# Performance work log

Hardware: AMD Instinct MI355X
Metric: run time of the kernel (lower is better)

## Reference

```python
import jax, jax.numpy as jnp
import numpy as np

TEMPERATURE = 0.07


def setup_inputs() -> dict:
    key = jax.random.key(0)
    k1, k2, k3 = jax.random.split(key, 3)
    B, V, D = 512, 1, 512
    features = jax.random.normal(k1, (B, V, D), dtype=jnp.float32)
    mask = jax.random.randint(k2, (B, B), 0, 2).astype(jnp.float32)
    mask_sents = jax.random.randint(k3, (B,), 0, 2).astype(jnp.bool_)
    return {"features": features, "mask": mask, "mask_sents": mask_sents}


def reference(features, mask, mask_sents):
    # features: [B, 1, D]; mask: [B, B] (0/1); mask_sents: [B] bool anchor selector
    B = features.shape[0]
    anchor = features[:, 0]                     # contrast_count == 1 -> anchor == contrast
    sim = jnp.matmul(anchor, anchor.T) / TEMPERATURE   # [B, B]

    logits_mask = 1.0 - jnp.eye(B, dtype=sim.dtype)    # zero out self-comparison
    sel = mask_sents.astype(sim.dtype)[:, None]        # weight instead of boolean row-select
    mask_pos = mask * logits_mask * sel                # [B, B]
    mask_neg = (1.0 - mask) * logits_mask * sel        # [B, B]

    # 'pre' branch: sum over rows i and (pos p, neg n) pairs of -logsigmoid(sim[i,p]-sim[i,n])
    diff = sim[:, :, None] - sim[:, None, :]           # [B, P, N] pairwise differences
    neg_logsig = -jax.nn.log_sigmoid(diff)
    loss_sum = jnp.einsum('ipn,ip,in->', neg_logsig, mask_pos, mask_neg)
    pair_num = jnp.sum(mask_pos.sum(1) * mask_neg.sum(1))
    loss = jnp.where(pair_num > 0, loss_sum / jnp.maximum(pair_num, 1.0), loss_sum)
    return loss
```

## Files before the change

kernel.cpp:

```cpp
#include <hip/hip_runtime.h>
#include <hip/hip_bf16.h>
#include <math.h>

#define BDIM 512
#define DDIM 512
#define SPLIT 4

typedef __attribute__((ext_vector_type(8))) short bfrag;
typedef __attribute__((ext_vector_type(4))) float ffrag;

__global__ __launch_bounds__(256) void convert_bf16(const float* __restrict__ A,
                                                    __hip_bfloat16* __restrict__ Ab,
                                                    double* __restrict__ acc) {
    const int idx = (blockIdx.x * 256 + threadIdx.x) * 4;
    if (idx == 0) { acc[0] = 0.0; acc[1] = 0.0; }
    float4 v = *(const float4*)&A[idx];
    union { __hip_bfloat16 h[4]; ushort4 u; } cv;
    cv.h[0] = __float2bfloat16(v.x); cv.h[1] = __float2bfloat16(v.y);
    cv.h[2] = __float2bfloat16(v.z); cv.h[3] = __float2bfloat16(v.w);
    *(ushort4*)&Ab[idx] = cv.u;
}

__global__ __launch_bounds__(256) void gemm_mfma(const __hip_bfloat16* __restrict__ Ab,
                                                 float* __restrict__ S) {
    const int tid = threadIdx.x;
    const int w = tid >> 6, lane = tid & 63;
    const int quad = lane >> 4, r = lane & 15;
    const int m0 = blockIdx.y * 64 + w * 16;
    const int n0 = blockIdx.x * 16;
    const __hip_bfloat16* arow = Ab + (m0 + r) * DDIM + quad * 8;
    const __hip_bfloat16* brow = Ab + (n0 + r) * DDIM + quad * 8;
    ffrag acc = {0.f, 0.f, 0.f, 0.f};
#pragma unroll
    for (int k = 0; k < DDIM; k += 32) {
        bfrag af = *(const bfrag*)(arow + k);
        bfrag bf = *(const bfrag*)(brow + k);
        acc = __builtin_amdgcn_mfma_f32_16x16x32_bf16(af, bf, acc, 0, 0, 0);
    }
    const float sc = 1.0f / 0.07f;
#pragma unroll
    for (int rg = 0; rg < 4; ++rg)
        S[(m0 + quad * 4 + rg) * BDIM + n0 + r] = acc[rg] * sc;
}

__device__ __forceinline__ float softplus_f(float z) {
    return fmaxf(z, 0.0f) + __logf(1.0f + __expf(-fabsf(z)));
}

__global__ __launch_bounds__(256) void pair_loss(const float* __restrict__ S,
                                                 const float* __restrict__ mask,
                                                 const int* __restrict__ sel,
                                                 double* __restrict__ acc) {
    const int i = blockIdx.x >> 2;
    const int q = blockIdx.x & 3;
    if (sel[i] == 0) return;
    __shared__ float sm[BDIM];
    __shared__ __align__(16) float ps[BDIM + 4];
    __shared__ float ns[BDIM];
    __shared__ int cnt[2];
    __shared__ float wsum[4];
    const int tid = threadIdx.x;
    const int lane = tid & 63, wave = tid >> 6;
    if (tid < 2) cnt[tid] = 0;
    for (int p = tid; p < BDIM; p += 256) sm[p] = S[i * BDIM + p];
    __syncthreads();
#pragma unroll
    for (int r = 0; r < 2; ++r) {
        const int p = tid + r * 256;
        const float m = mask[i * BDIM + p];
        const bool ok  = (p != i);
        const bool isp = ok && (m != 0.0f);
        const bool isn = ok && (m == 0.0f);
        unsigned long long bp = __ballot(isp);
        unsigned long long bn = __ballot(isn);
        unsigned long long lower = (1ULL << lane) - 1ULL;
        int pbase = 0, nbase = 0;
        if (lane == 0) {
            pbase = atomicAdd(&cnt[0], __popcll(bp));
            nbase = atomicAdd(&cnt[1], __popcll(bn));
        }
        pbase = __shfl(pbase, 0, 64);
        nbase = __shfl(nbase, 0, 64);
        if (isp) ps[pbase + __popcll(bp & lower)] = sm[p];
        if (isn) ns[nbase + __popcll(bn & lower)] = sm[p];
    }
    __syncthreads();
    const int npos = cnt[0], nneg = cnt[1];
    if (tid < 4) ps[npos + tid] = INFINITY;
    __syncthreads();
    int p0 = (q == 0) ? 0 : min(npos, ((q * npos) / SPLIT + 3) & ~3);
    int p1 = (q == SPLIT - 1) ? npos : min(npos, (((q + 1) * npos) / SPLIT + 3) & ~3);
    float l0 = 0.f, l1 = 0.f, l2 = 0.f, l3 = 0.f;
    for (int pp = p0; pp < p1; pp += 4) {
        float4 sp = *(const float4*)&ps[pp];
        for (int nn = tid; nn < nneg; nn += 256) {
            float sn = ns[nn];
            l0 += softplus_f(sn - sp.x);
            l1 += softplus_f(sn - sp.y);
            l2 += softplus_f(sn - sp.z);
            l3 += softplus_f(sn - sp.w);
        }
    }
    float local = (l0 + l1) + (l2 + l3);
#pragma unroll
    for (int off = 32; off > 0; off >>= 1) local += __shfl_down(local, off, 64);
    if (lane == 0) wsum[wave] = local;
    __syncthreads();
    if (tid == 0) {
        double tot = (double)wsum[0] + (double)wsum[1] + (double)wsum[2] + (double)wsum[3];
        atomicAdd(&acc[0], tot);
        if (q == 0) atomicAdd(&acc[1], (double)npos * (double)nneg);
    }
}

__global__ void finalize(const double* __restrict__ acc, float* __restrict__ out) {
    double ls = acc[0], pn = acc[1];
    double loss = (pn > 0.0) ? ls / fmax(pn, 1.0) : ls;
    out[0] = (float)loss;
}

extern "C" void kernel_launch(void* const* d_in, const int* in_sizes, int n_in,
                              void* d_out, int out_size, void* d_ws, size_t ws_size,
                              hipStream_t stream) {
    const float* feat = (const float*)d_in[0];
    const float* mask = (const float*)d_in[1];
    const int*   sel  = (const int*)d_in[2];
    float* out = (float*)d_out;

    char* ws = (char*)d_ws;
    float* S = (float*)ws;
    double* acc = (double*)(ws + BDIM * BDIM * sizeof(float));
    __hip_bfloat16* Ab = (__hip_bfloat16*)(ws + BDIM * BDIM * 4 + 1024);

    convert_bf16<<<BDIM * DDIM / 1024, 256, 0, stream>>>(feat, Ab, acc);
    gemm_mfma<<<dim3(BDIM / 16, BDIM / 64), 256, 0, stream>>>(Ab, S);
    pair_loss<<<BDIM * SPLIT, 256, 0, stream>>>(S, mask, sel, acc);
    finalize<<<1, 1, 0, stream>>>(acc, out);
}
```

Before: 88.62 us.

## Fuse bf16 conversion into GEMM and finalize into pair-loss via last-block counter

The separate fp32-to-bf16 conversion kernel is removed; the GEMM now loads fp32 features directly and converts them in registers before each MFMA. The finalize kernel is also removed: every pair_loss block increments an atomic counter, and the last block to finish computes the final loss. This cuts the launch count from four to two, trading away launch overhead and the intermediate bf16 buffer. In exchange the GEMM reads twice as many bytes, repeats the conversion for every tile, and every block now does an extra global atomic and a fence.

```diff
diff --git a/kernel.cpp b/kernel.cpp
--- a/kernel.cpp
+++ b/kernel.cpp
@@ -9,38 +9,41 @@
 typedef __attribute__((ext_vector_type(8))) short bfrag;
 typedef __attribute__((ext_vector_type(4))) float ffrag;
 
-__global__ __launch_bounds__(256) void convert_bf16(const float* __restrict__ A,
-                                                    __hip_bfloat16* __restrict__ Ab,
-                                                    double* __restrict__ acc) {
-    const int idx = (blockIdx.x * 256 + threadIdx.x) * 4;
-    if (idx == 0) { acc[0] = 0.0; acc[1] = 0.0; }
-    float4 v = *(const float4*)&A[idx];
-    union { __hip_bfloat16 h[4]; ushort4 u; } cv;
-    cv.h[0] = __float2bfloat16(v.x); cv.h[1] = __float2bfloat16(v.y);
-    cv.h[2] = __float2bfloat16(v.z); cv.h[3] = __float2bfloat16(v.w);
-    *(ushort4*)&Ab[idx] = cv.u;
+__device__ __forceinline__ bfrag cvt8(const float* __restrict__ p) {
+    float4 a = *(const float4*)p;
+    float4 b = *(const float4*)(p + 4);
+    union { __hip_bfloat16 h[8]; bfrag f; } u;
+    u.h[0] = __float2bfloat16(a.x); u.h[1] = __float2bfloat16(a.y);
+    u.h[2] = __float2bfloat16(a.z); u.h[3] = __float2bfloat16(a.w);
+    u.h[4] = __float2bfloat16(b.x); u.h[5] = __float2bfloat16(b.y);
+    u.h[6] = __float2bfloat16(b.z); u.h[7] = __float2bfloat16(b.w);
+    return u.f;
 }
 
-__global__ __launch_bounds__(256) void gemm_mfma(const __hip_bfloat16* __restrict__ Ab,
-                                                 float* __restrict__ S) {
+__global__ __launch_bounds__(256) void gemm_fused(const float* __restrict__ A,
+                                                  float* __restrict__ S,
+                                                  double* __restrict__ acc) {
+    if ((blockIdx.x | blockIdx.y) == 0 && threadIdx.x == 0) {
+        acc[0] = 0.0; acc[1] = 0.0;
+        *(unsigned*)(acc + 2) = 0u;
+    }
     const int tid = threadIdx.x;
     const int w = tid >> 6, lane = tid & 63;
     const int quad = lane >> 4, r = lane & 15;
     const int m0 = blockIdx.y * 64 + w * 16;
     const int n0 = blockIdx.x * 16;
-    const __hip_bfloat16* arow = Ab + (m0 + r) * DDIM + quad * 8;
-    const __hip_bfloat16* brow = Ab + (n0 + r) * DDIM + quad * 8;
-    ffrag acc = {0.f, 0.f, 0.f, 0.f};
+    const float* arow = A + (m0 + r) * DDIM + quad * 8;
+    const float* brow = A + (n0 + r) * DDIM + quad * 8;
+    ffrag c = {0.f, 0.f, 0.f, 0.f};
 #pragma unroll
     for (int k = 0; k < DDIM; k += 32) {
-        bfrag af = *(const bfrag*)(arow + k);
-        bfrag bf = *(const bfrag*)(brow + k);
-        acc = __builtin_amdgcn_mfma_f32_16x16x32_bf16(af, bf, acc, 0, 0, 0);
+        c = __builtin_amdgcn_mfma_f32_16x16x32_bf16(cvt8(arow + k), cvt8(brow + k),
+                                                    c, 0, 0, 0);
     }
     const float sc = 1.0f / 0.07f;
 #pragma unroll
     for (int rg = 0; rg < 4; ++rg)
-        S[(m0 + quad * 4 + rg) * BDIM + n0 + r] = acc[rg] * sc;
+        S[(m0 + quad * 4 + rg) * BDIM + n0 + r] = c[rg] * sc;
 }
 
 __device__ __forceinline__ float softplus_f(float z) {
@@ -50,73 +53,79 @@
 __global__ __launch_bounds__(256) void pair_loss(const float* __restrict__ S,
                                                  const float* __restrict__ mask,
                                                  const int* __restrict__ sel,
-                                                 double* __restrict__ acc) {
+                                                 double* __restrict__ acc,
+                                                 float* __restrict__ out) {
     const int i = blockIdx.x >> 2;
     const int q = blockIdx.x & 3;
-    if (sel[i] == 0) return;
-    __shared__ float sm[BDIM];
-    __shared__ __align__(16) float ps[BDIM + 4];
-    __shared__ float ns[BDIM];
-    __shared__ int cnt[2];
-    __shared__ float wsum[4];
     const int tid = threadIdx.x;
-    const int lane = tid & 63, wave = tid >> 6;
-    if (tid < 2) cnt[tid] = 0;
-    for (int p = tid; p < BDIM; p += 256) sm[p] = S[i * BDIM + p];
-    __syncthreads();
+    if (sel[i] != 0) {
+        __shared__ float sm[BDIM];
+        __shared__ __align__(16) float ps[BDIM + 4];
+        __shared__ float ns[BDIM];
+        __shared__ int cnt[2];
+        __shared__ float wsum[4];
+        const int lane = tid & 63, wave = tid >> 6;
+        if (tid < 2) cnt[tid] = 0;
+        for (int p = tid; p < BDIM; p += 256) sm[p] = S[i * BDIM + p];
+        __syncthreads();
 #pragma unroll
-    for (int r = 0; r < 2; ++r) {
-        const int p = tid + r * 256;
-        const float m = mask[i * BDIM + p];
-        const bool ok  = (p != i);
-        const bool isp = ok && (m != 0.0f);
-        const bool isn = ok && (m == 0.0f);
-        unsigned long long bp = __ballot(isp);
-        unsigned long long bn = __ballot(isn);
-        unsigned long long lower = (1ULL << lane) - 1ULL;
-        int pbase = 0, nbase = 0;
-        if (lane == 0) {
-            pbase = atomicAdd(&cnt[0], __popcll(bp));
-            nbase = atomicAdd(&cnt[1], __popcll(bn));
+        for (int r = 0; r < 2; ++r) {
+            const int p = tid + r * 256;
+            const float m = mask[i * BDIM + p];
+            const bool ok  = (p != i);
+            const bool isp = ok && (m != 0.0f);
+            const bool isn = ok && (m == 0.0f);
+            unsigned long long bp = __ballot(isp);
+            unsigned long long bn = __ballot(isn);
+            unsigned long long lower = (1ULL << lane) - 1ULL;
+            int pbase = 0, nbase = 0;
+            if (lane == 0) {
+                pbase = atomicAdd(&cnt[0], __popcll(bp));
+                nbase = atomicAdd(&cnt[1], __popcll(bn));
+            }
+            pbase = __shfl(pbase, 0, 64);
+            nbase = __shfl(nbase, 0, 64);
+            if (isp) ps[pbase + __popcll(bp & lower)] = sm[p];
+            if (isn) ns[nbase + __popcll(bn & lower)] = sm[p];
         }
-        pbase = __shfl(pbase, 0, 64);
-        nbase = __shfl(nbase, 0, 64);
-        if (isp) ps[pbase + __popcll(bp & lower)] = sm[p];
-        if (isn) ns[nbase + __popcll(bn & lower)] = sm[p];
-    }
-    __syncthreads();
-    const int npos = cnt[0], nneg = cnt[1];
-    if (tid < 4) ps[npos + tid] = INFINITY;
-    __syncthreads();
-    int p0 = (q == 0) ? 0 : min(npos, ((q * npos) / SPLIT + 3) & ~3);
-    int p1 = (q == SPLIT - 1) ? npos : min(npos, (((q + 1) * npos) / SPLIT + 3) & ~3);
-    float l0 = 0.f, l1 = 0.f, l2 = 0.f, l3 = 0.f;
-    for (int pp = p0; pp < p1; pp += 4) {
-        float4 sp = *(const float4*)&ps[pp];
-        for (int nn = tid; nn < nneg; nn += 256) {
-            float sn = ns[nn];
-            l0 += softplus_f(sn - sp.x);
-            l1 += softplus_f(sn - sp.y);
-            l2 += softplus_f(sn - sp.z);
-            l3 += softplus_f(sn - sp.w);
+        __syncthreads();
+        const int npos = cnt[0], nneg = cnt[1];
+        if (tid < 4) ps[npos + tid] = INFINITY;
+        __syncthreads();
+        int p0 = (q == 0) ? 0 : min(npos, ((q * npos) / SPLIT + 3) & ~3);
+        int p1 = (q == SPLIT - 1) ? npos : min(npos, (((q + 1) * npos) / SPLIT + 3) & ~3);
+        float l0 = 0.f, l1 = 0.f, l2 = 0.f, l3 = 0.f;
+        for (int pp = p0; pp < p1; pp += 4) {
+            float4 sp = *(const float4*)&ps[pp];
+            for (int nn = tid; nn < nneg; nn += 256) {
+                float sn = ns[nn];
+                l0 += softplus_f(sn - sp.x);
+                l1 += softplus_f(sn - sp.y);
+                l2 += softplus_f(sn - sp.z);
+                l3 += softplus_f(sn - sp.w);
+            }
+        }
+        float local = (l0 + l1) + (l2 + l3);
+#pragma unroll
+        for (int off = 32; off > 0; off >>= 1) local += __shfl_down(local, off, 64);
+        if (lane == 0) wsum[wave] = local;
+        __syncthreads();
+        if (tid == 0) {
+            double tot = (double)wsum[0] + (double)wsum[1] + (double)wsum[2] + (double)wsum[3];
+            atomicAdd(&acc[0], tot);
+            if (q == 0) atomicAdd(&acc[1], (double)npos * (double)nneg);
         }
     }
-    float local = (l0 + l1) + (l2 + l3);
-#pragma unroll
-    for (int off = 32; off > 0; off >>= 1) local += __shfl_down(local, off, 64);
-    if (lane == 0) wsum[wave] = local;
-    __syncthreads();
     if (tid == 0) {
-        double tot = (double)wsum[0] + (double)wsum[1] + (double)wsum[2] + (double)wsum[3];
-        atomicAdd(&acc[0], tot);
-        if (q == 0) atomicAdd(&acc[1], (double)npos * (double)nneg);
+        __threadfence();
+        unsigned t = atomicAdd((unsigned*)(acc + 2), 1u);
+        if (t == gridDim.x - 1) {
+            double ls = atomicAdd(&acc[0], 0.0);
+            double pn = atomicAdd(&acc[1], 0.0);
+            double loss = (pn > 0.0) ? ls / fmax(pn, 1.0) : ls;
+            out[0] = (float)loss;
+        }
     }
-}
-
-__global__ void finalize(const double* __restrict__ acc, float* __restrict__ out) {
-    double ls = acc[0], pn = acc[1];
-    double loss = (pn > 0.0) ? ls / fmax(pn, 1.0) : ls;
-    out[0] = (float)loss;
 }
 
 extern "C" void kernel_launch(void* const* d_in, const int* in_sizes, int n_in,
@@ -130,10 +139,7 @@
     char* ws = (char*)d_ws;
     float* S = (float*)ws;
     double* acc = (double*)(ws + BDIM * BDIM * sizeof(float));
-    __hip_bfloat16* Ab = (__hip_bfloat16*)(ws + BDIM * BDIM * 4 + 1024);
 
-    convert_bf16<<<BDIM * DDIM / 1024, 256, 0, stream>>>(feat, Ab, acc);
-    gemm_mfma<<<dim3(BDIM / 16, BDIM / 64), 256, 0, stream>>>(Ab, S);
-    pair_loss<<<BDIM * SPLIT, 256, 0, stream>>>(S, mask, sel, acc);
-    finalize<<<1, 1, 0, stream>>>(acc, out);
+    gemm_fused<<<dim3(BDIM / 16, BDIM / 64), 256, 0, stream>>>(feat, S, acc);
+    pair_loss<<<BDIM * SPLIT, 256, 0, stream>>>(S, mask, sel, acc, out);
 }
```

Measured after the change: 119.4 us. +34.7%, slower.
